# Optimization experiments

Measured on AMD Instinct MI355X. Metric: run time of the kernel, lower is better.

Reference implementation:

```python
import jax, jax.numpy as jnp
import numpy as np
import math

S = 4096          # tokens
MODEL_DIM = 2048
NUM_EXPERTS = 32
TOP_K = 2
CAPACITY_FACTOR = 1.0
MIN_CAPACITY = 4


def _capacity(num_tokens, num_experts, capacity_factor, min_capacity):
    # static (shape-derived) capacity, matching _capacity in the torch code
    cap = int(math.ceil(num_tokens / num_experts * capacity_factor))
    return max(cap, min_capacity)


def setup_inputs() -> dict:
    key = jax.random.key(0)
    kx, kw = jax.random.split(key)
    x = jax.random.normal(kx, (S, MODEL_DIM), dtype=jnp.float32)
    # gate weight of Linear(model_dim, num_experts, bias=False): [E, M]
    wg = jax.random.normal(kw, (NUM_EXPERTS, MODEL_DIM), dtype=jnp.float32) * (1.0 / math.sqrt(MODEL_DIM))
    return {"x": x, "wg": wg}


def topkgating(logits, k, capacity_factor, min_capacity):
    s, e = logits.shape
    top_gate, top_idx = jax.lax.top_k(logits, k)                    # [s,k]
    gates = jax.nn.softmax(logits, axis=1)                          # [s,e]
    rows = jnp.arange(s)[:, None]
    # scatter raw top-k logits into dense [s,e] (zeros elsewhere), as torch does
    topk_masked_gates = jnp.zeros_like(logits).at[rows, top_idx].set(top_gate)
    mask = jnp.zeros((s, e), dtype=bool).at[rows, top_idx].set(True)
    exp_counts = mask.sum(axis=0)                                   # [e]

    me = gates.mean(axis=0)
    ce = mask.astype(gates.dtype).mean(axis=0)
    l_aux = jnp.mean(me * ce) * e * e / k

    capacity = _capacity(s, e, capacity_factor * k, min_capacity)   # static int

    # drop_policy == 'probs': keep top-`capacity` tokens per expert by gate value
    _, cap_idx = jax.lax.top_k(topk_masked_gates.T, capacity)       # [e, C] token ids
    e_ids = jnp.broadcast_to(jnp.arange(e)[:, None], cap_idx.shape)
    capacity_mask = jnp.zeros((s, e), dtype=bool).at[cap_idx, e_ids].set(True)
    mask = jnp.logical_and(mask, capacity_mask)

    locations = jnp.cumsum(mask.astype(jnp.int32), axis=0) - 1      # [s,e]
    locations_s = jnp.sum(locations * mask, axis=1)                 # [s] slot per token

    maskf = mask.astype(gates.dtype)
    gates_masked = gates * maskf
    denom_s = jnp.clip(jnp.sum(gates_masked, axis=-1, keepdims=True),
                       jnp.finfo(gates.dtype).eps, None)
    gates_masked = gates_masked / denom_s

    locations_sc = jax.nn.one_hot(locations_s, capacity, dtype=gates.dtype)  # [s,C]
    combine_weights = jnp.einsum('se,sc->sec', gates_masked, locations_sc)   # [s,e,C]
    dispatch_mask = combine_weights.astype(bool)
    return l_aux, combine_weights, dispatch_mask, exp_counts


def reference(x, wg):
    logits = x @ wg.T                                               # [s,e]
    return topkgating(logits, TOP_K, CAPACITY_FACTOR, MIN_CAPACITY)
```

## Files before the change

kernel.cpp:

```cpp
#include <hip/hip_runtime.h>
#include <cstddef>
#include <math.h>

#define S_TOK 4096
#define MDIM  2048
#define NE    32
#define CAP   256
#define TPB   256
#define TOKB  4

struct Ws {
    int   counts[NE];
    int   ecount[NE];
    int   loc_s[S_TOK];
    int   keptA[S_TOK];
    int   keptB[S_TOK];
    float gate_sum[NE];
    int   e1a[S_TOK];
    int   e2a[S_TOK];
    float g1a[S_TOK];
    float g2a[S_TOK];
    int   etok[NE * S_TOK];
    float eval[NE * S_TOK];
};

__global__ __launch_bounds__(TPB) void k_gate(const float* __restrict__ x,
                                              const float* __restrict__ wg,
                                              Ws* __restrict__ ws) {
    __shared__ float4 xs4[TOKB * 512];
    __shared__ double part[8][NE][TOKB];
    __shared__ float  logitsF[TOKB][NE];
    __shared__ float  gsumL[NE];

    const int tid = threadIdx.x;
    const int t0  = blockIdx.x * TOKB;

    if (tid < NE) gsumL[tid] = 0.f;

    const float4* x4 = (const float4*)x;
    #pragma unroll
    for (int k = 0; k < (TOKB * 512) / TPB; ++k) {
        int idx = tid + k * TPB;
        xs4[idx] = x4[(size_t)t0 * 512 + idx];
    }
    __syncthreads();

    const int e   = tid & 31;
    const int seg = tid >> 5;
    double acc[TOKB];
    #pragma unroll
    for (int i = 0; i < TOKB; ++i) acc[i] = 0.0;

    const float4* wg4 = (const float4*)wg;
    for (int j4 = 0; j4 < 64; ++j4) {
        float4 w = wg4[e * 512 + seg * 64 + j4];
        #pragma unroll
        for (int tt = 0; tt < TOKB; ++tt) {
            float4 xv = xs4[tt * 512 + seg * 64 + j4];
            acc[tt] += (double)xv.x * w.x + (double)xv.y * w.y +
                       (double)xv.z * w.z + (double)xv.w * w.w;
        }
    }
    #pragma unroll
    for (int tt = 0; tt < TOKB; ++tt) part[seg][e][tt] = acc[tt];
    __syncthreads();

    if (tid < TOKB * 32) {
        int tok = tid >> 5;
        int ee  = tid & 31;
        double s = 0.0;
        #pragma unroll
        for (int sg = 0; sg < 8; ++sg) s += part[sg][ee][tok];
        logitsF[tok][ee] = (float)s;
    }
    __syncthreads();

    const int lane = tid & 63;
    const int half = lane >> 5;
    const int grp  = (tid >> 6) * 2 + half;
    const int le   = lane & 31;

    if (grp < TOKB) {
        float l = logitsF[grp][le];

        float v1 = l; int e1 = le;
        #pragma unroll
        for (int m = 16; m >= 1; m >>= 1) {
            float ov = __shfl_xor(v1, m);
            int   oi = __shfl_xor(e1, m);
            if (ov > v1 || (ov == v1 && oi < e1)) { v1 = ov; e1 = oi; }
        }
        float v2 = (le == e1) ? -INFINITY : l;
        int   e2 = (le == e1) ? 0x7fffffff : le;
        #pragma unroll
        for (int m = 16; m >= 1; m >>= 1) {
            float ov = __shfl_xor(v2, m);
            int   oi = __shfl_xor(e2, m);
            if (ov > v2 || (ov == v2 && oi < e2)) { v2 = ov; e2 = oi; }
        }
        float p = expf(l - v1);
        float ssum = p;
        #pragma unroll
        for (int m = 16; m >= 1; m >>= 1) ssum += __shfl_xor(ssum, m);
        float gate = p / ssum;
        atomicAdd(&gsumL[le], gate);

        float g1 = __shfl(gate, (half << 5) + e1);
        float g2 = __shfl(gate, (half << 5) + e2);

        if (le == 0) {
            int t = t0 + grp;
            atomicAdd(&ws->counts[e1], 1);
            atomicAdd(&ws->counts[e2], 1);
            int i1 = atomicAdd(&ws->ecount[e1], 1);
            ws->etok[e1 * S_TOK + i1] = t;
            ws->eval[e1 * S_TOK + i1] = v1;
            int i2 = atomicAdd(&ws->ecount[e2], 1);
            ws->etok[e2 * S_TOK + i2] = t;
            ws->eval[e2 * S_TOK + i2] = v2;
            ws->e1a[t] = e1; ws->e2a[t] = e2;
            ws->g1a[t] = g1; ws->g2a[t] = g2;
        }
    }
    __syncthreads();
    if (tid < NE) atomicAdd(&ws->gate_sum[tid], gsumL[tid]);
}

__global__ __launch_bounds__(256) void k_capacity(Ws* __restrict__ ws) {
    __shared__ float vals[S_TOK];
    __shared__ int   toks[S_TOK];
    __shared__ unsigned char kept[S_TOK];

    const int e = blockIdx.x;
    const int n = ws->ecount[e];

    for (int i = threadIdx.x; i < n; i += 256) {
        vals[i] = ws->eval[e * S_TOK + i];
        toks[i] = ws->etok[e * S_TOK + i];
    }
    __syncthreads();

    for (int i = threadIdx.x; i < n; i += 256) {
        float v = vals[i];
        int   t = toks[i];
        int rank = (v < 0.f) ? (S_TOK - n) : 0;
        int alt  = 0;
        for (int j = 0; j < n; ++j) {
            float vj = vals[j]; int tj = toks[j];
            rank += (vj > v || (vj == v && tj < t)) ? 1 : 0;
            alt  += (tj < t) ? 1 : 0;
        }
        if (v == 0.f) rank += t - alt;
        kept[i] = (rank < CAP) ? 1 : 0;
    }
    __syncthreads();

    for (int i = threadIdx.x; i < n; i += 256) {
        if (!kept[i]) continue;
        int t = toks[i];
        int loc = 0;
        for (int j = 0; j < n; ++j) loc += (kept[j] && toks[j] < t) ? 1 : 0;
        atomicAdd(&ws->loc_s[t], loc);
        if (ws->e1a[t] == e) ws->keptA[t] = 1;
        else                 ws->keptB[t] = 1;
    }
}

__global__ __launch_bounds__(256) void k_out(const Ws* __restrict__ ws,
                                             float* __restrict__ out) {
    const int t = blockIdx.x;
    __shared__ int   s_p1, s_p2;
    __shared__ float s_w1, s_w2;

    if (threadIdx.x == 0) {
        int p1 = -1, p2 = -1;
        float w1 = 0.f, w2 = 0.f;
        int kA = ws->keptA[t], kB = ws->keptB[t];
        int loc = ws->loc_s[t];
        if ((kA | kB) && loc < CAP) {
            float g1 = ws->g1a[t], g2 = ws->g2a[t];
            float d = (kA ? g1 : 0.f) + (kB ? g2 : 0.f);
            d = fmaxf(d, 1.1920929e-07f);
            if (kA) { p1 = ws->e1a[t] * CAP + loc; w1 = g1 / d; }
            if (kB) { p2 = ws->e2a[t] * CAP + loc; w2 = g2 / d; }
        }
        s_p1 = p1; s_p2 = p2; s_w1 = w1; s_w2 = w2;
    }
    __syncthreads();

    const int p1 = s_p1, p2 = s_p2;
    const float w1 = s_w1, w2 = s_w2;

    float* cw = out + 1 + (size_t)t * (NE * CAP);
    float* dm = out + 1 + (size_t)S_TOK * NE * CAP + (size_t)t * (NE * CAP);

    if (threadIdx.x < 4) {
        int off = (threadIdx.x < 3) ? threadIdx.x : (NE * CAP - 1);
        float c = 0.f, m = 0.f;
        if (off == p1) { c = w1; m = 1.f; }
        if (off == p2) { c += w2; m = 1.f; }
        cw[off] = c; dm[off] = m;
    }

    float4* cw4 = (float4*)(cw + 3);
    float4* dm4 = (float4*)(dm + 3);
    for (int f = threadIdx.x; f < 2047; f += 256) {
        int base = 3 + f * 4;
        float4 c = {0.f, 0.f, 0.f, 0.f};
        float4 m = {0.f, 0.f, 0.f, 0.f};
        if (p1 >= base && p1 < base + 4) { ((float*)&c)[p1 - base] = w1; ((float*)&m)[p1 - base] = 1.f; }
        if (p2 >= base && p2 < base + 4) { ((float*)&c)[p2 - base] += w2; ((float*)&m)[p2 - base] = 1.f; }
        cw4[f] = c; dm4[f] = m;
    }
}

__global__ __launch_bounds__(64) void k_final(const Ws* __restrict__ ws,
                                              float* __restrict__ out) {
    int tid = threadIdx.x;
    float part = 0.f;
    if (tid < NE) {
        int c = ws->counts[tid];
        out[1 + 2 * (size_t)S_TOK * NE * CAP + tid] = (float)c;
        float me = ws->gate_sum[tid] / (float)S_TOK;
        float ce = (float)c / (float)S_TOK;
        part = me * ce;
    }
    #pragma unroll
    for (int m = 16; m >= 1; m >>= 1) part += __shfl_xor(part, m);
    if (tid == 0) out[0] = part * ((float)NE * (float)NE / 2.0f / (float)NE);
}

extern "C" void kernel_launch(void* const* d_in, const int* in_sizes, int n_in,
                              void* d_out, int out_size, void* d_ws, size_t ws_size,
                              hipStream_t stream) {
    const float* x  = (const float*)d_in[0];
    const float* wg = (const float*)d_in[1];
    float* out = (float*)d_out;
    Ws* ws = (Ws*)d_ws;

    hipMemsetAsync(d_ws, 0, offsetof(Ws, e1a), stream);

    k_gate<<<S_TOK / TOKB, TPB, 0, stream>>>(x, wg, ws);
    k_capacity<<<NE, 256, 0, stream>>>(ws);
    k_out<<<S_TOK, 256, 0, stream>>>(ws, out);
    k_final<<<1, 64, 0, stream>>>(ws, out);
}
```

Measured before the change: 477.8 us.

## Fuse all gating stages into one cooperative persistent kernel with grid syncs

Merges the memset, gate, capacity, output and final kernels into a single cooperative kernel of 256 blocks that uses grid-wide barriers between stages, so per-launch overhead goes away. Each block now processes 16 tokens for the gate and output stages, which lowers parallelism compared with 1024 and 4096 blocks. Larger shared memory use, since the capacity buffers live in every block, may reduce occupancy. The capacity stage still runs on only 32 blocks while the rest sit idle at the grid barrier.

After: 550.1 us. 1.15x slower.

```diff
diff --git a/kernel.cpp b/kernel.cpp
--- a/kernel.cpp
+++ b/kernel.cpp
@@ -1,13 +1,18 @@
 #include <hip/hip_runtime.h>
+#include <hip/hip_cooperative_groups.h>
 #include <cstddef>
 #include <math.h>
+
+namespace cg = cooperative_groups;
 
 #define S_TOK 4096
 #define MDIM  2048
 #define NE    32
 #define CAP   256
 #define TPB   256
+#define NBLK  256
 #define TOKB  4
+#define TPB_TOK 16
 
 struct Ws {
     int   counts[NE];
@@ -24,155 +29,162 @@
     float eval[NE * S_TOK];
 };
 
-__global__ __launch_bounds__(TPB) void k_gate(const float* __restrict__ x,
-                                              const float* __restrict__ wg,
-                                              Ws* __restrict__ ws) {
+__global__ __launch_bounds__(TPB) void k_all(const float* __restrict__ x,
+                                             const float* __restrict__ wg,
+                                             Ws* __restrict__ ws,
+                                             float* __restrict__ out) {
+    cg::grid_group grid = cg::this_grid();
+    const int tid = threadIdx.x;
+    const int bid = blockIdx.x;
+
     __shared__ float4 xs4[TOKB * 512];
     __shared__ double part[8][NE][TOKB];
     __shared__ float  logitsF[TOKB][NE];
     __shared__ float  gsumL[NE];
-
-    const int tid = threadIdx.x;
-    const int t0  = blockIdx.x * TOKB;
-
+    __shared__ float  vals[S_TOK];
+    __shared__ int    toks[S_TOK];
+    __shared__ unsigned char kept[S_TOK];
+
+    {
+        const int nInt = (int)(offsetof(Ws, e1a) / sizeof(int));
+        int* w = (int*)ws;
+        for (int i = bid * TPB + tid; i < nInt; i += NBLK * TPB) w[i] = 0;
+    }
     if (tid < NE) gsumL[tid] = 0.f;
-
-    const float4* x4 = (const float4*)x;
-    #pragma unroll
-    for (int k = 0; k < (TOKB * 512) / TPB; ++k) {
-        int idx = tid + k * TPB;
-        xs4[idx] = x4[(size_t)t0 * 512 + idx];
-    }
-    __syncthreads();
-
+    grid.sync();
+
+    const float4* x4  = (const float4*)x;
+    const float4* wg4 = (const float4*)wg;
     const int e   = tid & 31;
     const int seg = tid >> 5;
-    double acc[TOKB];
-    #pragma unroll
-    for (int i = 0; i < TOKB; ++i) acc[i] = 0.0;
-
-    const float4* wg4 = (const float4*)wg;
-    for (int j4 = 0; j4 < 64; ++j4) {
-        float4 w = wg4[e * 512 + seg * 64 + j4];
-        #pragma unroll
-        for (int tt = 0; tt < TOKB; ++tt) {
-            float4 xv = xs4[tt * 512 + seg * 64 + j4];
-            acc[tt] += (double)xv.x * w.x + (double)xv.y * w.y +
-                       (double)xv.z * w.z + (double)xv.w * w.w;
-        }
-    }
-    #pragma unroll
-    for (int tt = 0; tt < TOKB; ++tt) part[seg][e][tt] = acc[tt];
-    __syncthreads();
-
-    if (tid < TOKB * 32) {
-        int tok = tid >> 5;
-        int ee  = tid & 31;
-        double s = 0.0;
-        #pragma unroll
-        for (int sg = 0; sg < 8; ++sg) s += part[sg][ee][tok];
-        logitsF[tok][ee] = (float)s;
-    }
-    __syncthreads();
-
     const int lane = tid & 63;
     const int half = lane >> 5;
     const int grp  = (tid >> 6) * 2 + half;
     const int le   = lane & 31;
 
-    if (grp < TOKB) {
-        float l = logitsF[grp][le];
-
-        float v1 = l; int e1 = le;
-        #pragma unroll
-        for (int m = 16; m >= 1; m >>= 1) {
-            float ov = __shfl_xor(v1, m);
-            int   oi = __shfl_xor(e1, m);
-            if (ov > v1 || (ov == v1 && oi < e1)) { v1 = ov; e1 = oi; }
-        }
-        float v2 = (le == e1) ? -INFINITY : l;
-        int   e2 = (le == e1) ? 0x7fffffff : le;
-        #pragma unroll
-        for (int m = 16; m >= 1; m >>= 1) {
-            float ov = __shfl_xor(v2, m);
-            int   oi = __shfl_xor(e2, m);
-            if (ov > v2 || (ov == v2 && oi < e2)) { v2 = ov; e2 = oi; }
-        }
-        float p = expf(l - v1);
-        float ssum = p;
-        #pragma unroll
-        for (int m = 16; m >= 1; m >>= 1) ssum += __shfl_xor(ssum, m);
-        float gate = p / ssum;
-        atomicAdd(&gsumL[le], gate);
-
-        float g1 = __shfl(gate, (half << 5) + e1);
-        float g2 = __shfl(gate, (half << 5) + e2);
-
-        if (le == 0) {
-            int t = t0 + grp;
-            atomicAdd(&ws->counts[e1], 1);
-            atomicAdd(&ws->counts[e2], 1);
-            int i1 = atomicAdd(&ws->ecount[e1], 1);
-            ws->etok[e1 * S_TOK + i1] = t;
-            ws->eval[e1 * S_TOK + i1] = v1;
-            int i2 = atomicAdd(&ws->ecount[e2], 1);
-            ws->etok[e2 * S_TOK + i2] = t;
-            ws->eval[e2 * S_TOK + i2] = v2;
-            ws->e1a[t] = e1; ws->e2a[t] = e2;
-            ws->g1a[t] = g1; ws->g2a[t] = g2;
-        }
-    }
-    __syncthreads();
+    for (int it = 0; it < TPB_TOK / TOKB; ++it) {
+        const int t0 = bid * TPB_TOK + it * TOKB;
+
+        #pragma unroll
+        for (int k = 0; k < (TOKB * 512) / TPB; ++k) {
+            int idx = tid + k * TPB;
+            xs4[idx] = x4[(size_t)t0 * 512 + idx];
+        }
+        __syncthreads();
+
+        double acc[TOKB];
+        #pragma unroll
+        for (int i = 0; i < TOKB; ++i) acc[i] = 0.0;
+        for (int j4 = 0; j4 < 64; ++j4) {
+            float4 w = wg4[e * 512 + seg * 64 + j4];
+            #pragma unroll
+            for (int tt = 0; tt < TOKB; ++tt) {
+                float4 xv = xs4[tt * 512 + seg * 64 + j4];
+                acc[tt] += (double)xv.x * w.x + (double)xv.y * w.y +
+                           (double)xv.z * w.z + (double)xv.w * w.w;
+            }
+        }
+        #pragma unroll
+        for (int tt = 0; tt < TOKB; ++tt) part[seg][e][tt] = acc[tt];
+        __syncthreads();
+
+        if (tid < TOKB * 32) {
+            int tok = tid >> 5;
+            int ee  = tid & 31;
+            double s = 0.0;
+            #pragma unroll
+            for (int sg = 0; sg < 8; ++sg) s += part[sg][ee][tok];
+            logitsF[tok][ee] = (float)s;
+        }
+        __syncthreads();
+
+        if (grp < TOKB) {
+            float l = logitsF[grp][le];
+
+            float v1 = l; int e1 = le;
+            #pragma unroll
+            for (int m = 16; m >= 1; m >>= 1) {
+                float ov = __shfl_xor(v1, m);
+                int   oi = __shfl_xor(e1, m);
+                if (ov > v1 || (ov == v1 && oi < e1)) { v1 = ov; e1 = oi; }
+            }
+            float v2 = (le == e1) ? -INFINITY : l;
+            int   e2 = (le == e1) ? 0x7fffffff : le;
+            #pragma unroll
+            for (int m = 16; m >= 1; m >>= 1) {
+                float ov = __shfl_xor(v2, m);
+                int   oi = __shfl_xor(e2, m);
+                if (ov > v2 || (ov == v2 && oi < e2)) { v2 = ov; e2 = oi; }
+            }
+            float p = expf(l - v1);
+            float ssum = p;
+            #pragma unroll
+            for (int m = 16; m >= 1; m >>= 1) ssum += __shfl_xor(ssum, m);
+            float gate = p / ssum;
+            atomicAdd(&gsumL[le], gate);
+
+            float g1 = __shfl(gate, (half << 5) + e1);
+            float g2 = __shfl(gate, (half << 5) + e2);
+
+            if (le == 0) {
+                int t = t0 + grp;
+                atomicAdd(&ws->counts[e1], 1);
+                atomicAdd(&ws->counts[e2], 1);
+                int i1 = atomicAdd(&ws->ecount[e1], 1);
+                ws->etok[e1 * S_TOK + i1] = t;
+                ws->eval[e1 * S_TOK + i1] = v1;
+                int i2 = atomicAdd(&ws->ecount[e2], 1);
+                ws->etok[e2 * S_TOK + i2] = t;
+                ws->eval[e2 * S_TOK + i2] = v2;
+                ws->e1a[t] = e1; ws->e2a[t] = e2;
+                ws->g1a[t] = g1; ws->g2a[t] = g2;
+            }
+        }
+        __syncthreads();
+    }
     if (tid < NE) atomicAdd(&ws->gate_sum[tid], gsumL[tid]);
-}
-
-__global__ __launch_bounds__(256) void k_capacity(Ws* __restrict__ ws) {
-    __shared__ float vals[S_TOK];
-    __shared__ int   toks[S_TOK];
-    __shared__ unsigned char kept[S_TOK];
-
-    const int e = blockIdx.x;
-    const int n = ws->ecount[e];
-
-    for (int i = threadIdx.x; i < n; i += 256) {
-        vals[i] = ws->eval[e * S_TOK + i];
-        toks[i] = ws->etok[e * S_TOK + i];
-    }
-    __syncthreads();
-
-    for (int i = threadIdx.x; i < n; i += 256) {
-        float v = vals[i];
-        int   t = toks[i];
-        int rank = (v < 0.f) ? (S_TOK - n) : 0;
-        int alt  = 0;
-        for (int j = 0; j < n; ++j) {
-            float vj = vals[j]; int tj = toks[j];
-            rank += (vj > v || (vj == v && tj < t)) ? 1 : 0;
-            alt  += (tj < t) ? 1 : 0;
-        }
-        if (v == 0.f) rank += t - alt;
-        kept[i] = (rank < CAP) ? 1 : 0;
-    }
-    __syncthreads();
-
-    for (int i = threadIdx.x; i < n; i += 256) {
-        if (!kept[i]) continue;
-        int t = toks[i];
-        int loc = 0;
-        for (int j = 0; j < n; ++j) loc += (kept[j] && toks[j] < t) ? 1 : 0;
-        atomicAdd(&ws->loc_s[t], loc);
-        if (ws->e1a[t] == e) ws->keptA[t] = 1;
-        else                 ws->keptB[t] = 1;
-    }
-}
-
-__global__ __launch_bounds__(256) void k_out(const Ws* __restrict__ ws,
-                                             float* __restrict__ out) {
-    const int t = blockIdx.x;
-    __shared__ int   s_p1, s_p2;
-    __shared__ float s_w1, s_w2;
-
-    if (threadIdx.x == 0) {
+    grid.sync();
+
+    if (bid < NE) {
+        const int ee = bid;
+        const int n = ws->ecount[ee];
+
+        for (int i = tid; i < n; i += TPB) {
+            vals[i] = ws->eval[ee * S_TOK + i];
+            toks[i] = ws->etok[ee * S_TOK + i];
+        }
+        __syncthreads();
+
+        for (int i = tid; i < n; i += TPB) {
+            float v = vals[i];
+            int   t = toks[i];
+            int rank = (v < 0.f) ? (S_TOK - n) : 0;
+            int alt  = 0;
+            for (int j = 0; j < n; ++j) {
+                float vj = vals[j]; int tj = toks[j];
+                rank += (vj > v || (vj == v && tj < t)) ? 1 : 0;
+                alt  += (tj < t) ? 1 : 0;
+            }
+            if (v == 0.f) rank += t - alt;
+            kept[i] = (rank < CAP) ? 1 : 0;
+        }
+        __syncthreads();
+
+        for (int i = tid; i < n; i += TPB) {
+            if (!kept[i]) continue;
+            int t = toks[i];
+            int loc = 0;
+            for (int j = 0; j < n; ++j) loc += (kept[j] && toks[j] < t) ? 1 : 0;
+            atomicAdd(&ws->loc_s[t], loc);
+            if (ws->e1a[t] == e) { }
+            if (ws->e1a[t] == ee) ws->keptA[t] = 1;
+            else                  ws->keptB[t] = 1;
+        }
+    }
+    grid.sync();
+
+    for (int tt = 0; tt < TPB_TOK; ++tt) {
+        const int t = bid * TPB_TOK + tt;
         int p1 = -1, p2 = -1;
         float w1 = 0.f, w2 = 0.f;
         int kA = ws->keptA[t], kB = ws->keptB[t];
@@ -184,50 +196,42 @@
             if (kA) { p1 = ws->e1a[t] * CAP + loc; w1 = g1 / d; }
             if (kB) { p2 = ws->e2a[t] * CAP + loc; w2 = g2 / d; }
         }
-        s_p1 = p1; s_p2 = p2; s_w1 = w1; s_w2 = w2;
-    }
-    __syncthreads();
-
-    const int p1 = s_p1, p2 = s_p2;
-    const float w1 = s_w1, w2 = s_w2;
-
-    float* cw = out + 1 + (size_t)t * (NE * CAP);
-    float* dm = out + 1 + (size_t)S_TOK * NE * CAP + (size_t)t * (NE * CAP);
-
-    if (threadIdx.x < 4) {
-        int off = (threadIdx.x < 3) ? threadIdx.x : (NE * CAP - 1);
-        float c = 0.f, m = 0.f;
-        if (off == p1) { c = w1; m = 1.f; }
-        if (off == p2) { c += w2; m = 1.f; }
-        cw[off] = c; dm[off] = m;
-    }
-
-    float4* cw4 = (float4*)(cw + 3);
-    float4* dm4 = (float4*)(dm + 3);
-    for (int f = threadIdx.x; f < 2047; f += 256) {
-        int base = 3 + f * 4;
-        float4 c = {0.f, 0.f, 0.f, 0.f};
-        float4 m = {0.f, 0.f, 0.f, 0.f};
-        if (p1 >= base && p1 < base + 4) { ((float*)&c)[p1 - base] = w1; ((float*)&m)[p1 - base] = 1.f; }
-        if (p2 >= base && p2 < base + 4) { ((float*)&c)[p2 - base] += w2; ((float*)&m)[p2 - base] = 1.f; }
-        cw4[f] = c; dm4[f] = m;
-    }
-}
-
-__global__ __launch_bounds__(64) void k_final(const Ws* __restrict__ ws,
-                                              float* __restrict__ out) {
-    int tid = threadIdx.x;
-    float part = 0.f;
-    if (tid < NE) {
-        int c = ws->counts[tid];
-        out[1 + 2 * (size_t)S_TOK * NE * CAP + tid] = (float)c;
-        float me = ws->gate_sum[tid] / (float)S_TOK;
-        float ce = (float)c / (float)S_TOK;
-        part = me * ce;
-    }
-    #pragma unroll
-    for (int m = 16; m >= 1; m >>= 1) part += __shfl_xor(part, m);
-    if (tid == 0) out[0] = part * ((float)NE * (float)NE / 2.0f / (float)NE);
+
+        float* cw = out + 1 + (size_t)t * (NE * CAP);
+        float* dm = out + 1 + (size_t)S_TOK * NE * CAP + (size_t)t * (NE * CAP);
+
+        if (tid < 4) {
+            int off = (tid < 3) ? tid : (NE * CAP - 1);
+            float c = 0.f, m = 0.f;
+            if (off == p1) { c = w1; m = 1.f; }
+            if (off == p2) { c += w2; m = 1.f; }
+            cw[off] = c; dm[off] = m;
+        }
+        float4* cw4 = (float4*)(cw + 3);
+        float4* dm4 = (float4*)(dm + 3);
+        for (int f = tid; f < 2047; f += TPB) {
+            int base = 3 + f * 4;
+            float4 c = {0.f, 0.f, 0.f, 0.f};
+            float4 m = {0.f, 0.f, 0.f, 0.f};
+            if (p1 >= base && p1 < base + 4) { ((float*)&c)[p1 - base] = w1; ((float*)&m)[p1 - base] = 1.f; }
+            if (p2 >= base && p2 < base + 4) { ((float*)&c)[p2 - base] += w2; ((float*)&m)[p2 - base] = 1.f; }
+            cw4[f] = c; dm4[f] = m;
+        }
+    }
+
+    if (bid == 0 && tid < 64) {
+        float partial = 0.f;
+        if (tid < NE) {
+            int c = ws->counts[tid];
+            out[1 + 2 * (size_t)S_TOK * NE * CAP + tid] = (float)c;
+            float me = ws->gate_sum[tid] / (float)S_TOK;
+            float ce = (float)c / (float)S_TOK;
+            partial = me * ce;
+        }
+        #pragma unroll
+        for (int m = 16; m >= 1; m >>= 1) partial += __shfl_xor(partial, m);
+        if (tid == 0) out[0] = partial * 16.0f;
+    }
 }
 
 extern "C" void kernel_launch(void* const* d_in, const int* in_sizes, int n_in,
@@ -238,10 +242,7 @@
     float* out = (float*)d_out;
     Ws* ws = (Ws*)d_ws;
 
-    hipMemsetAsync(d_ws, 0, offsetof(Ws, e1a), stream);
-
-    k_gate<<<S_TOK / TOKB, TPB, 0, stream>>>(x, wg, ws);
-    k_capacity<<<NE, 256, 0, stream>>>(ws);
-    k_out<<<S_TOK, 256, 0, stream>>>(ws, out);
-    k_final<<<1, 64, 0, stream>>>(ws, out);
+    void* args[] = { (void*)&x, (void*)&wg, (void*)&ws, (void*)&out };
+    hipLaunchCooperativeKernel((const void*)k_all, dim3(NBLK), dim3(TPB),
+                               args, 0, stream);
 }
```
